# Kernel tuning notes

Hardware: AMD Instinct MI355X
Metric: run time of the kernel (lower is better)

## Reference

```python
import jax, jax.numpy as jnp
import numpy as np

HEAD_DIM = 128
ROPE_THETA = 500000.0  # Llama3
NEG_INF = -1e9


def _apply_rope(t, cos, sin):
    # t: [b, s, h, d]; cos/sin: [s, d//2]
    b, s, h, d = t.shape
    tr = t.reshape(b, s, h, d // 2, 2)
    xr, xi = tr[..., 0], tr[..., 1]
    c = cos[None, :, None, :]
    sn = sin[None, :, None, :]
    out = jnp.stack([xr * c - xi * sn, xr * sn + xi * c], axis=-1)
    return out.reshape(b, s, h, d)


def setup_inputs() -> dict:
    key = jax.random.key(0)
    ks = jax.random.split(key, 8)
    bsz, seqlen, model_dim = 2, 2048, 4096
    n_heads, n_kv_heads, head_dim = 32, 8, HEAD_DIM
    max_bsz, max_seqlen = 2, 4096
    pos = 0

    x = jax.random.normal(ks[0], (bsz, seqlen, model_dim), dtype=jnp.float32)
    wq = jax.random.normal(ks[1], (model_dim, n_heads * head_dim), dtype=jnp.float32) * 0.02
    wk = jax.random.normal(ks[2], (model_dim, n_kv_heads * head_dim), dtype=jnp.float32) * 0.02
    wv = jax.random.normal(ks[3], (model_dim, n_kv_heads * head_dim), dtype=jnp.float32) * 0.02
    wo = jax.random.normal(ks[4], (n_heads * head_dim, model_dim), dtype=jnp.float32) * 0.02

    # RoPE tables for positions [pos, pos+seqlen)
    inv_freq = 1.0 / (ROPE_THETA ** (jnp.arange(0, head_dim, 2, dtype=jnp.float32) / head_dim))
    t = jnp.arange(pos, pos + seqlen, dtype=jnp.float32)
    ang = jnp.outer(t, inv_freq)  # [s, d//2]
    freqs_cos, freqs_sin = jnp.cos(ang), jnp.sin(ang)

    # causal additive mask over cached length (pos + seqlen)
    q_idx = jnp.arange(seqlen)[:, None] + pos
    k_idx = jnp.arange(pos + seqlen)[None, :]
    mask = jnp.where(k_idx <= q_idx, 0.0, NEG_INF).astype(jnp.float32)

    k_cache = jnp.zeros((max_bsz, max_seqlen, n_kv_heads, head_dim), dtype=jnp.float32)
    v_cache = jnp.zeros((max_bsz, max_seqlen, n_kv_heads, head_dim), dtype=jnp.float32)
    return {"x": x, "pos": pos, "freqs_cos": freqs_cos, "freqs_sin": freqs_sin,
            "mask": mask, "wq": wq, "wk": wk, "wv": wv, "wo": wo,
            "k_cache": k_cache, "v_cache": v_cache}


def reference(x, pos, freqs_cos, freqs_sin, mask, wq, wk, wv, wo, k_cache, v_cache):
    bsz, seqlen, _ = x.shape
    head_dim = 2 * freqs_cos.shape[-1]
    n_heads = wq.shape[1] // head_dim
    n_kv_heads = wk.shape[1] // head_dim

    q = (x @ wq).reshape(bsz, seqlen, n_heads, head_dim)
    k = (x @ wk).reshape(bsz, seqlen, n_kv_heads, head_dim)
    v = (x @ wv).reshape(bsz, seqlen, n_kv_heads, head_dim)

    q = _apply_rope(q, freqs_cos, freqs_sin)
    k = _apply_rope(k, freqs_cos, freqs_sin)

    # KV-cache append then read back [:, :pos+seqlen]
    k_cache = k_cache.at[:bsz, pos:pos + seqlen].set(k)
    v_cache = v_cache.at[:bsz, pos:pos + seqlen].set(v)
    keys = k_cache[:bsz, :pos + seqlen]      # [b, kv_len, n_kv, d]
    values = v_cache[:bsz, :pos + seqlen]

    repeats = n_heads // n_kv_heads
    keys = jnp.repeat(keys, repeats, axis=2)     # [b, kv_len, h, d]
    values = jnp.repeat(values, repeats, axis=2)

    scale = 1.0 / jnp.sqrt(jnp.float32(head_dim))
    scores = jnp.einsum('bqhd,bkhd->bhqk', q, keys) * scale + mask
    attn = jax.nn.softmax(scores, axis=-1)
    out = jnp.einsum('bhqk,bkhd->bqhd', attn, values)
    out = out.reshape(bsz, seqlen, n_heads * head_dim)
    return out @ wo
```

## Files before the change

kernel.cpp:

```cpp
#include <hip/hip_runtime.h>
#include <hip/hip_bf16.h>

typedef __bf16 bf16x8 __attribute__((ext_vector_type(8)));
typedef float  f32x4  __attribute__((ext_vector_type(4)));

#define DEVI __device__ __forceinline__

DEVI void async_copy16(const void* g, void* s) {
  __builtin_amdgcn_global_load_lds(
      (__attribute__((address_space(1))) void*)g,
      (__attribute__((address_space(3))) void*)s,
      16, 0, 0);
}

DEVI unsigned pack_bf16x2(float lo, float hi) {
  union { __hip_bfloat16 h[2]; unsigned u; } pk;
  pk.h[0] = __float2bfloat16(lo);
  pk.h[1] = __float2bfloat16(hi);
  return pk.u;
}

__global__ __launch_bounds__(256) void cvt_f32_bf16(const float* __restrict__ in,
                                                    __hip_bfloat16* __restrict__ out,
                                                    int n) {
  int i = (blockIdx.x * 256 + threadIdx.x) * 4;
  if (i >= n) return;
  float4 v = *(const float4*)(in + i);
  union { __hip_bfloat16 h[4]; ushort4 u; } o;
  o.h[0] = __float2bfloat16(v.x);
  o.h[1] = __float2bfloat16(v.y);
  o.h[2] = __float2bfloat16(v.z);
  o.h[3] = __float2bfloat16(v.w);
  *(ushort4*)(out + i) = o.u;
}

__global__ __launch_bounds__(256) void transpose_cvt(const float* __restrict__ W,
                                                     __hip_bfloat16* __restrict__ WT,
                                                     int Kdim, int Ndim) {
  __shared__ float tile[32][33];
  int bx = blockIdx.x * 32;
  int by = blockIdx.y * 32;
  int tx = threadIdx.x;
  int ty = threadIdx.y;
  #pragma unroll
  for (int j = 0; j < 32; j += 8)
    tile[ty + j][tx] = W[(size_t)(by + ty + j) * Ndim + bx + tx];
  __syncthreads();
  #pragma unroll
  for (int j = 0; j < 32; j += 8)
    WT[(size_t)(bx + ty + j) * Kdim + by + tx] = __float2bfloat16(tile[tx][ty + j]);
}

__global__ __launch_bounds__(256) void transpose_v(const __hip_bfloat16* __restrict__ vb,
                                                   __hip_bfloat16* __restrict__ vt) {
  __shared__ __hip_bfloat16 tile[32][33];
  const int s0 = blockIdx.x * 32, d0 = blockIdx.y * 32;
  const int bk = blockIdx.z;
  const int bb = bk >> 3, kvh = bk & 7;
  const int tx = threadIdx.x, ty = threadIdx.y;
  #pragma unroll
  for (int j = 0; j < 32; j += 8)
    tile[ty + j][tx] =
        vb[((size_t)(bb * 2048 + s0 + ty + j) * 8 + kvh) * 128 + d0 + tx];
  __syncthreads();
  #pragma unroll
  for (int j = 0; j < 32; j += 8)
    vt[((size_t)bk * 128 + d0 + ty + j) * 2048 + s0 + tx] = tile[tx][ty + j];
}

template <int EPI>
__global__ __launch_bounds__(256) void gemm_bt(
    const __hip_bfloat16* __restrict__ A,
    const __hip_bfloat16* __restrict__ BT,
    float* __restrict__ Cf,
    __hip_bfloat16* __restrict__ Cb,
    __hip_bfloat16* __restrict__ Cb2,
    int M, int N, int K,
    const float* __restrict__ fcos,
    const float* __restrict__ fsin,
    float scale) {
  __shared__ alignas(16) __hip_bfloat16 lds[3][8192];
  const int tid = threadIdx.x;
  const int w = tid >> 6, l = tid & 63;
  const int l4 = l >> 4, l15 = l & 15;
  const int wr = w >> 1, wc = w & 1;
  const int rowBase = blockIdx.y * 128;
  const int colBase = blockIdx.x * 128;

  const __hip_bfloat16* aSrc[2];
  const __hip_bfloat16* bSrc[2];
  int dstOff[2];
  #pragma unroll
  for (int i = 0; i < 2; i++) {
    int c = i * 256 + tid;
    int r = c >> 2;
    int kb = (c & 3) ^ ((r >> 1) & 3);
    aSrc[i] = A  + (size_t)(rowBase + r) * K + kb * 8;
    bSrc[i] = BT + (size_t)(colBase + r) * K + kb * 8;
    dstOff[i] = (i * 256 + w * 64) * 16;
  }

  f32x4 acc[4][4];
  #pragma unroll
  for (int mi = 0; mi < 4; mi++)
    #pragma unroll
    for (int ni = 0; ni < 4; ni++)
      acc[mi][ni] = (f32x4){0.f, 0.f, 0.f, 0.f};

  #pragma unroll
  for (int i = 0; i < 2; i++) {
    async_copy16(aSrc[i], (char*)lds + dstOff[i]);
    async_copy16(bSrc[i], (char*)lds + 8192 + dstOff[i]);
  }
  #pragma unroll
  for (int i = 0; i < 2; i++) {
    async_copy16(aSrc[i] + 32, (char*)lds + 16384 + dstOff[i]);
    async_copy16(bSrc[i] + 32, (char*)lds + 16384 + 8192 + dstOff[i]);
  }

  int cur = 0;
  for (int k0 = 0; k0 < K; k0 += 32) {
    if (k0 + 32 < K) {
      asm volatile("s_waitcnt vmcnt(4)" ::: "memory");
    } else {
      asm volatile("s_waitcnt vmcnt(0)" ::: "memory");
    }
    __builtin_amdgcn_s_barrier();
    __builtin_amdgcn_sched_barrier(0);

    const char* base = (const char*)lds + cur * 16384;
    bf16x8 aF[4], bF[4];
    #pragma unroll
    for (int mi = 0; mi < 4; mi++) {
      int row = wr * 64 + mi * 16 + l15;
      int phys = l4 ^ ((row >> 1) & 3);
      aF[mi] = *(const bf16x8*)(base + row * 64 + phys * 16);
    }
    #pragma unroll
    for (int ni = 0; ni < 4; ni++) {
      int row = wc * 64 + ni * 16 + l15;
      int phys = l4 ^ ((row >> 1) & 3);
      bF[ni] = *(const bf16x8*)(base + 8192 + row * 64 + phys * 16);
    }
    asm volatile("s_waitcnt lgkmcnt(0)" ::: "memory");
    __builtin_amdgcn_sched_barrier(0);

    if (k0 + 64 < K) {
      int nxt = cur + 2; if (nxt >= 3) nxt -= 3;
      #pragma unroll
      for (int i = 0; i < 2; i++) {
        async_copy16(aSrc[i] + k0 + 64, (char*)lds + nxt * 16384 + dstOff[i]);
        async_copy16(bSrc[i] + k0 + 64, (char*)lds + nxt * 16384 + 8192 + dstOff[i]);
      }
    }

    __builtin_amdgcn_s_setprio(1);
    #pragma unroll
    for (int mi = 0; mi < 4; mi++)
      #pragma unroll
      for (int ni = 0; ni < 4; ni++)
        acc[mi][ni] = __builtin_amdgcn_mfma_f32_16x16x32_bf16(aF[mi], bF[ni], acc[mi][ni], 0, 0, 0);
    __builtin_amdgcn_s_setprio(0);
    cur = (cur + 1 == 3) ? 0 : cur + 1;
  }

  const int orow0 = rowBase + wr * 64 + l4 * 4;
  const int ocol0 = colBase + wc * 64 + l15;
  #pragma unroll
  for (int mi = 0; mi < 4; mi++) {
    #pragma unroll
    for (int ni = 0; ni < 4; ni++) {
      #pragma unroll
      for (int reg = 0; reg < 4; reg++) {
        int r = orow0 + mi * 16 + reg;
        int col = ocol0 + ni * 16;
        float v = acc[mi][ni][reg];
        if constexpr (EPI == 0) {
          Cf[(size_t)r * N + col] = v;
        } else if constexpr (EPI == 1) {
          Cb[(size_t)r * N + col] = __float2bfloat16(v * scale);
        } else if constexpr (EPI == 2) {
          float p = __shfl_xor(v, 1);
          int dd = col & 127;
          int fi = dd >> 1;
          int srow = r & 2047;
          float c = fcos[srow * 64 + fi];
          float s = fsin[srow * 64 + fi];
          float outv = ((col & 1) == 0) ? (v * c - p * s) : (p * s + v * c);
          Cb[(size_t)r * N + col] = __float2bfloat16(outv * scale);
        } else {
          if (colBase < 1024) {
            float p = __shfl_xor(v, 1);
            int dd = col & 127;
            int fi = dd >> 1;
            int srow = r & 2047;
            float c = fcos[srow * 64 + fi];
            float s = fsin[srow * 64 + fi];
            float outv = ((col & 1) == 0) ? (v * c - p * s) : (p * s + v * c);
            Cb[(size_t)r * 1024 + col] = __float2bfloat16(outv);
          } else {
            Cb2[(size_t)r * 1024 + (col - 1024)] = __float2bfloat16(v);
          }
        }
      }
    }
  }
}

__global__ __launch_bounds__(256, 2) void attn_kernel(
    const __hip_bfloat16* __restrict__ Q,
    const __hip_bfloat16* __restrict__ Kb,
    const __hip_bfloat16* __restrict__ Vt_g,
    __hip_bfloat16* __restrict__ O) {
  const int S = 2048, HD = 4096, KVD = 1024, D = 128;
  const int h = blockIdx.y, b = blockIdx.z;
  const int kvh = h >> 2;
  const int bk = b * 8 + kvh;
  const int tid = threadIdx.x;
  const int w = tid >> 6, l = tid & 63;
  const int l4 = l >> 4, l15 = l & 15;

  __shared__ alignas(16) __hip_bfloat16 Kt[2][64 * 128];
  __shared__ alignas(16) __hip_bfloat16 Vt[2][128 * 64];
  __shared__ alignas(16) __hip_bfloat16 Pb[4 * 32 * 64];

  const __hip_bfloat16* kSrc[4];
  const __hip_bfloat16* vSrc[4];
  int stDst[4];
  #pragma unroll
  for (int i = 0; i < 4; i++) {
    int c = i * 256 + tid;
    int kr = c >> 4;
    int kds = (c & 15) ^ (kr & 7);
    kSrc[i] = Kb + (size_t)(b * S + kr) * KVD + kvh * D + kds * 8;
    int vr = c >> 3;
    int vds = (c & 7) ^ (vr & 7);
    vSrc[i] = Vt_g + ((size_t)bk * 128 + vr) * 2048 + vds * 8;
    stDst[i] = (i * 256 + w * 64) * 16;
  }

  char* pbase = (char*)Pb + w * 4096;

  for (int pass = 0; pass < 2; pass++) {
    const int qt = pass ? (15 - blockIdx.x) : blockIdx.x;
    const int qbase = qt * 128 + w * 32;
    const int nt = 2 * qt + 2;

    bf16x8 qf[2][4];
    #pragma unroll
    for (int f = 0; f < 2; f++) {
      const int qrow = qbase + f * 16 + l15;
      const __hip_bfloat16* qptr = Q + (size_t)(b * S + qrow) * HD + h * D + l4 * 8;
      #pragma unroll
      for (int dc = 0; dc < 4; dc++) qf[f][dc] = *(const bf16x8*)(qptr + dc * 32);
    }

    f32x4 o[2][8];
    #pragma unroll
    for (int f = 0; f < 2; f++)
      #pragma unroll
      for (int nf = 0; nf < 8; nf++) o[f][nf] = (f32x4){0.f, 0.f, 0.f, 0.f};
    float mrun[2]  = {-1e30f, -1e30f};
    float llrun[2] = {0.f, 0.f};

    if (pass) __syncthreads();

    #pragma unroll
    for (int i = 0; i < 4; i++) {
      async_copy16(kSrc[i], (char*)Kt + stDst[i]);
      async_copy16(vSrc[i], (char*)Vt + stDst[i]);
    }

    int cur = 0;
    for (int t = 0; t < nt; t++) {
      __syncthreads();
      if (t + 1 < nt) {
        const int kv1 = (t + 1) * 64;
        #pragma unroll
        for (int i = 0; i < 4; i++) {
          async_copy16(kSrc[i] + (size_t)kv1 * KVD, (char*)Kt + (cur ^ 1) * 16384 + stDst[i]);
          async_copy16(vSrc[i] + kv1,               (char*)Vt + (cur ^ 1) * 16384 + stDst[i]);
        }
      }
      const char* ktb = (const char*)Kt + cur * 16384;
      const char* vtb = (const char*)Vt + cur * 16384;
      const int kv0 = t * 64;

      f32x4 s[2][4];
      #pragma unroll
      for (int f = 0; f < 2; f++)
        #pragma unroll
        for (int kg = 0; kg < 4; kg++) s[f][kg] = (f32x4){0.f, 0.f, 0.f, 0.f};
      __builtin_amdgcn_s_setprio(1);
      #pragma unroll
      for (int dc = 0; dc < 4; dc++) {
        #pragma unroll
        for (int kg = 0; kg < 4; kg++) {
          int key = kg * 16 + l15;
          int phys = (dc * 4 + l4) ^ (key & 7);
          bf16x8 kf = *(const bf16x8*)(ktb + key * 256 + phys * 16);
          s[0][kg] = __builtin_amdgcn_mfma_f32_16x16x32_bf16(kf, qf[0][dc], s[0][kg], 0, 0, 0);
          s[1][kg] = __builtin_amdgcn_mfma_f32_16x16x32_bf16(kf, qf[1][dc], s[1][kg], 0, 0, 0);
        }
      }
      __builtin_amdgcn_s_setprio(0);

      if (t >= nt - 2) {
        #pragma unroll
        for (int f = 0; f < 2; f++) {
          int q = qbase + f * 16 + l15;
          #pragma unroll
          for (int kg = 0; kg < 4; kg++)
            #pragma unroll
            for (int reg = 0; reg < 4; reg++)
              if (kv0 + kg * 16 + 4 * l4 + reg > q) s[f][kg][reg] = -1e30f;
        }
      }

      #pragma unroll
      for (int f = 0; f < 2; f++) {
        float pmax = -1e30f;
        #pragma unroll
        for (int kg = 0; kg < 4; kg++)
          #pragma unroll
          for (int reg = 0; reg < 4; reg++) pmax = fmaxf(pmax, s[f][kg][reg]);
        pmax = fmaxf(pmax, __shfl_xor(pmax, 16));
        pmax = fmaxf(pmax, __shfl_xor(pmax, 32));
        float mn = fmaxf(mrun[f], pmax);
        float alpha = __expf(mrun[f] - mn);
        mrun[f] = mn;
        float rs = 0.f;
        #pragma unroll
        for (int kg = 0; kg < 4; kg++)
          #pragma unroll
          for (int reg = 0; reg < 4; reg++) {
            float p = __expf(s[f][kg][reg] - mn);
            s[f][kg][reg] = p;
            rs += p;
          }
        rs += __shfl_xor(rs, 16);
        rs += __shfl_xor(rs, 32);
        llrun[f] = llrun[f] * alpha + rs;

        #pragma unroll
        for (int kg = 0; kg < 4; kg++)
          #pragma unroll
          for (int p2 = 0; p2 < 2; p2++) {
            unsigned u = pack_bf16x2(s[f][kg][2 * p2], s[f][kg][2 * p2 + 1]);
            int slot16 = 2 * kg + (l4 >> 1);
            int inner = (8 * l4 + 4 * p2) & 15;
            *(unsigned*)(pbase + (f * 16 + l15) * 128 + ((slot16 ^ (l15 & 7)) * 16) + inner) = u;
          }

        float alpha_r[4];
        #pragma unroll
        for (int reg = 0; reg < 4; reg++)
          alpha_r[reg] = __shfl(alpha, (l & 48) + 4 * l4 + reg);
        #pragma unroll
        for (int nf = 0; nf < 8; nf++)
          #pragma unroll
          for (int reg = 0; reg < 4; reg++) o[f][nf][reg] *= alpha_r[reg];
      }

      __builtin_amdgcn_s_setprio(1);
      #pragma unroll
      for (int half = 0; half < 2; half++) {
        int physp = (half * 4 + l4) ^ (l15 & 7);
        bf16x8 pa0 = *(const bf16x8*)(pbase + (0 * 16 + l15) * 128 + physp * 16);
        bf16x8 pa1 = *(const bf16x8*)(pbase + (1 * 16 + l15) * 128 + physp * 16);
        #pragma unroll
        for (int nf = 0; nf < 8; nf++) {
          int d = nf * 16 + l15;
          bf16x8 vf = *(const bf16x8*)(vtb + d * 128 + physp * 16);
          o[0][nf] = __builtin_amdgcn_mfma_f32_16x16x32_bf16(pa0, vf, o[0][nf], 0, 0, 0);
          o[1][nf] = __builtin_amdgcn_mfma_f32_16x16x32_bf16(pa1, vf, o[1][nf], 0, 0, 0);
        }
      }
      __builtin_amdgcn_s_setprio(0);
      cur ^= 1;
    }

    #pragma unroll
    for (int f = 0; f < 2; f++) {
      #pragma unroll
      for (int reg = 0; reg < 4; reg++) {
        float llr = __shfl(llrun[f], (l & 48) + 4 * l4 + reg);
        float inv = 1.0f / llr;
        int r = qbase + f * 16 + 4 * l4 + reg;
        __hip_bfloat16* optr = O + (size_t)(b * S + r) * HD + h * D + l15;
        #pragma unroll
        for (int nf = 0; nf < 8; nf++) optr[nf * 16] = __float2bfloat16(o[f][nf][reg] * inv);
      }
    }
  }
}

extern "C" void kernel_launch(void* const* d_in, const int* in_sizes, int n_in,
                              void* d_out, int out_size, void* d_ws, size_t ws_size,
                              hipStream_t stream) {
  const float* x    = (const float*)d_in[0];
  const float* fcos = (const float*)d_in[2];
  const float* fsin = (const float*)d_in[3];
  const float* wq   = (const float*)d_in[5];
  const float* wk   = (const float*)d_in[6];
  const float* wv   = (const float*)d_in[7];
  const float* wo   = (const float*)d_in[8];
  float* out = (float*)d_out;

  char* ws = (char*)d_ws;
  const size_t MB = 1024 * 1024;
  __hip_bfloat16* xb  = (__hip_bfloat16*)(ws + 0);
  __hip_bfloat16* wT  = (__hip_bfloat16*)(ws + 32 * MB);
  __hip_bfloat16* wkT = (__hip_bfloat16*)(ws + 64 * MB);
  __hip_bfloat16* wvT = (__hip_bfloat16*)(ws + 72 * MB);
  __hip_bfloat16* qb  = (__hip_bfloat16*)(ws + 80 * MB);
  __hip_bfloat16* kb  = (__hip_bfloat16*)(ws + 112 * MB);
  __hip_bfloat16* vb  = (__hip_bfloat16*)(ws + 120 * MB);
  __hip_bfloat16* ab  = xb;
  __hip_bfloat16* vt  = wT;

  const float qscale = 0.08838834764831845f;

  cvt_f32_bf16<<<16384, 256, 0, stream>>>(x, xb, 16777216);
  transpose_cvt<<<dim3(128, 128), dim3(32, 8), 0, stream>>>(wq, wT, 4096, 4096);
  transpose_cvt<<<dim3(32, 128), dim3(32, 8), 0, stream>>>(wk, wkT, 4096, 1024);
  transpose_cvt<<<dim3(32, 128), dim3(32, 8), 0, stream>>>(wv, wvT, 4096, 1024);

  gemm_bt<2><<<dim3(32, 32), 256, 0, stream>>>(xb, wT,  nullptr, qb, nullptr,
                                               4096, 4096, 4096, fcos, fsin, qscale);
  gemm_bt<3><<<dim3(16, 32), 256, 0, stream>>>(xb, wkT, nullptr, kb, vb,
                                               4096, 2048, 4096, fcos, fsin, 1.0f);

  transpose_v<<<dim3(64, 4, 16), dim3(32, 8), 0, stream>>>(vb, vt);

  attn_kernel<<<dim3(8, 32, 2), 256, 0, stream>>>(qb, kb, vt, ab);

  transpose_cvt<<<dim3(128, 128), dim3(32, 8), 0, stream>>>(wo, wT, 4096, 4096);
  gemm_bt<0><<<dim3(32, 32), 256, 0, stream>>>(ab, wT, out, nullptr, nullptr,
                                               4096, 4096, 4096, nullptr, nullptr, 1.0f);
}
```

Baseline: 580.6 us.

## Add 256x256-tile 8-wave GEMM with staged async prefetch for Q and output projections

Introduces a new GEMM kernel using 256x256 output tiles, 512 threads (8 waves), double-buffered 128 KB LDS with XOR swizzle, and prefetch of the next K-tile split into four chunks interleaved with MFMA phases. It replaces the 128-tile GEMM for the Q projection (with RoPE epilogue) and the output projection. Larger tiles raise operand reuse per global load and cut the block count to 256, which roughly matches the CU count, so each CU does fewer, heavier tiles. In exchange the accumulator count (128 floats per thread) raises register pressure. The 128 KB of LDS per block likely limits occupancy to one block per CU despite the launch bound of 2.

```diff
diff --git a/kernel.cpp b/kernel.cpp
--- a/kernel.cpp
+++ b/kernel.cpp
@@ -66,6 +66,178 @@
   #pragma unroll
   for (int j = 0; j < 32; j += 8)
     vt[((size_t)bk * 128 + d0 + ty + j) * 2048 + s0 + tx] = tile[tx][ty + j];
+}
+
+template <int EPI>
+__global__ __launch_bounds__(512, 2) void gemm256(
+    const __hip_bfloat16* __restrict__ A,
+    const __hip_bfloat16* __restrict__ BT,
+    float* __restrict__ Cf,
+    __hip_bfloat16* __restrict__ Cb,
+    int M, int N, int K,
+    const float* __restrict__ fcos,
+    const float* __restrict__ fsin,
+    float scale) {
+  __shared__ alignas(16) char lds[2][65536];
+  const int tid = threadIdx.x;
+  const int w = tid >> 6, l = tid & 63;
+  const int l4 = l >> 4, l15 = l & 15;
+  const int wr = w >> 2, wc = w & 3;
+  const int rowBase = blockIdx.y * 256;
+  const int colBase = blockIdx.x * 256;
+
+  const __hip_bfloat16* aS[2];
+  const __hip_bfloat16* bS[2];
+  int dstOff[2];
+  #pragma unroll
+  for (int i = 0; i < 2; i++) {
+    int c = i * 512 + tid;
+    int r = c >> 3;
+    int kb = (c & 7) ^ (r & 7);
+    aS[i] = A  + (size_t)(rowBase + r) * K + kb * 8;
+    bS[i] = BT + (size_t)(colBase + r) * K + kb * 8;
+    dstOff[i] = i * 8192 + w * 1024;
+  }
+  const size_t hstep = (size_t)128 * K;
+
+  f32x4 acc[8][4];
+  #pragma unroll
+  for (int mi = 0; mi < 8; mi++)
+    #pragma unroll
+    for (int ni = 0; ni < 4; ni++)
+      acc[mi][ni] = (f32x4){0.f, 0.f, 0.f, 0.f};
+
+  #pragma unroll
+  for (int i = 0; i < 2; i++) async_copy16(aS[i],         lds[0] + 0     + dstOff[i]);
+  #pragma unroll
+  for (int i = 0; i < 2; i++) async_copy16(aS[i] + hstep, lds[0] + 16384 + dstOff[i]);
+  #pragma unroll
+  for (int i = 0; i < 2; i++) async_copy16(bS[i],         lds[0] + 32768 + dstOff[i]);
+  #pragma unroll
+  for (int i = 0; i < 2; i++) async_copy16(bS[i] + hstep, lds[0] + 49152 + dstOff[i]);
+
+  const int NT = K >> 6;
+  const int pswz = l15 & 7;
+  bf16x8 bF[4][2];
+
+  for (int kt = 0; kt < NT; kt++) {
+    const char* bufc = lds[kt & 1];
+    char* bufn = lds[(kt & 1) ^ 1];
+    const int koff = (kt + 1) * 64;
+    const bool pre = (kt + 1 < NT);
+
+    if (pre) {
+      #pragma unroll
+      for (int i = 0; i < 2; i++) async_copy16(aS[i] + koff, bufn + 0 + dstOff[i]);
+    }
+    if (pre) { asm volatile("s_waitcnt vmcnt(2)" ::: "memory"); }
+    else     { asm volatile("s_waitcnt vmcnt(0)" ::: "memory"); }
+    __builtin_amdgcn_s_barrier();
+    __builtin_amdgcn_sched_barrier(0);
+
+    #pragma unroll
+    for (int ni = 0; ni < 4; ni++)
+      #pragma unroll
+      for (int kh = 0; kh < 2; kh++) {
+        int R = wc * 64 + ni * 16 + l15;
+        int phys = (kh * 4 + l4) ^ pswz;
+        bF[ni][kh] = *(const bf16x8*)(bufc + 32768 + (R >> 7) * 16384 +
+                                      (R & 127) * 128 + phys * 16);
+      }
+    {
+      bf16x8 aF[2][2];
+      #pragma unroll
+      for (int f = 0; f < 2; f++)
+        #pragma unroll
+        for (int kh = 0; kh < 2; kh++) {
+          int lr = f * 16 + l15;
+          int phys = (kh * 4 + l4) ^ pswz;
+          aF[f][kh] = *(const bf16x8*)(bufc + wr * 16384 + lr * 128 + phys * 16);
+        }
+      asm volatile("s_waitcnt lgkmcnt(0)" ::: "memory");
+      __builtin_amdgcn_sched_barrier(0);
+      __builtin_amdgcn_s_setprio(1);
+      #pragma unroll
+      for (int f = 0; f < 2; f++)
+        #pragma unroll
+        for (int ni = 0; ni < 4; ni++)
+          #pragma unroll
+          for (int kh = 0; kh < 2; kh++)
+            acc[f][ni] = __builtin_amdgcn_mfma_f32_16x16x32_bf16(
+                aF[f][kh], bF[ni][kh], acc[f][ni], 0, 0, 0);
+      __builtin_amdgcn_s_setprio(0);
+    }
+    __builtin_amdgcn_s_barrier();
+
+    #pragma unroll
+    for (int p = 1; p < 4; p++) {
+      bf16x8 aF[2][2];
+      #pragma unroll
+      for (int f = 0; f < 2; f++)
+        #pragma unroll
+        for (int kh = 0; kh < 2; kh++) {
+          int lr = (2 * p + f) * 16 + l15;
+          int phys = (kh * 4 + l4) ^ pswz;
+          aF[f][kh] = *(const bf16x8*)(bufc + wr * 16384 + lr * 128 + phys * 16);
+        }
+      if (pre) {
+        if (p == 1) {
+          #pragma unroll
+          for (int i = 0; i < 2; i++)
+            async_copy16(aS[i] + hstep + koff, bufn + 16384 + dstOff[i]);
+        } else if (p == 2) {
+          #pragma unroll
+          for (int i = 0; i < 2; i++)
+            async_copy16(bS[i] + koff, bufn + 32768 + dstOff[i]);
+        } else {
+          #pragma unroll
+          for (int i = 0; i < 2; i++)
+            async_copy16(bS[i] + hstep + koff, bufn + 49152 + dstOff[i]);
+        }
+      }
+      __builtin_amdgcn_s_barrier();
+      asm volatile("s_waitcnt lgkmcnt(0)" ::: "memory");
+      __builtin_amdgcn_sched_barrier(0);
+      __builtin_amdgcn_s_setprio(1);
+      #pragma unroll
+      for (int f = 0; f < 2; f++)
+        #pragma unroll
+        for (int ni = 0; ni < 4; ni++)
+          #pragma unroll
+          for (int kh = 0; kh < 2; kh++)
+            acc[2 * p + f][ni] = __builtin_amdgcn_mfma_f32_16x16x32_bf16(
+                aF[f][kh], bF[ni][kh], acc[2 * p + f][ni], 0, 0, 0);
+      __builtin_amdgcn_s_setprio(0);
+      __builtin_amdgcn_s_barrier();
+    }
+  }
+
+  const int orow0 = rowBase + wr * 128 + l4 * 4;
+  const int ocol0 = colBase + wc * 64 + l15;
+  #pragma unroll
+  for (int mi = 0; mi < 8; mi++) {
+    #pragma unroll
+    for (int ni = 0; ni < 4; ni++) {
+      #pragma unroll
+      for (int reg = 0; reg < 4; reg++) {
+        int r = orow0 + mi * 16 + reg;
+        int col = ocol0 + ni * 16;
+        float v = acc[mi][ni][reg];
+        if constexpr (EPI == 0) {
+          Cf[(size_t)r * N + col] = v;
+        } else {
+          float p2 = __shfl_xor(v, 1);
+          int dd = col & 127;
+          int fi = dd >> 1;
+          int srow = r & 2047;
+          float c = fcos[srow * 64 + fi];
+          float s = fsin[srow * 64 + fi];
+          float outv = ((col & 1) == 0) ? (v * c - p2 * s) : (p2 * s + v * c);
+          Cb[(size_t)r * N + col] = __float2bfloat16(outv * scale);
+        }
+      }
+    }
+  }
 }
 
 template <int EPI>
@@ -426,7 +598,7 @@
   transpose_cvt<<<dim3(32, 128), dim3(32, 8), 0, stream>>>(wk, wkT, 4096, 1024);
   transpose_cvt<<<dim3(32, 128), dim3(32, 8), 0, stream>>>(wv, wvT, 4096, 1024);
 
-  gemm_bt<2><<<dim3(32, 32), 256, 0, stream>>>(xb, wT,  nullptr, qb, nullptr,
+  gemm256<2><<<dim3(16, 16), 512, 0, stream>>>(xb, wT, nullptr, qb,
                                                4096, 4096, 4096, fcos, fsin, qscale);
   gemm_bt<3><<<dim3(16, 32), 256, 0, stream>>>(xb, wkT, nullptr, kb, vb,
                                                4096, 2048, 4096, fcos, fsin, 1.0f);
@@ -436,6 +608,6 @@
   attn_kernel<<<dim3(8, 32, 2), 256, 0, stream>>>(qb, kb, vt, ab);
 
   transpose_cvt<<<dim3(128, 128), dim3(32, 8), 0, stream>>>(wo, wT, 4096, 4096);
-  gemm_bt<0><<<dim3(32, 32), 256, 0, stream>>>(ab, wT, out, nullptr, nullptr,
+  gemm256<0><<<dim3(16, 16), 512, 0, stream>>>(ab, wT, out, nullptr,
                                                4096, 4096, 4096, nullptr, nullptr, 1.0f);
 }
```

New measurement: 514.4 us. 1.13x faster.
